# Kernel tuning notes

Measured on AMD Instinct MI355X. Metric: run time of the kernel, lower is better.

The kernel has to match this reference:

```python
import jax, jax.numpy as jnp
import numpy as np

LN_EPS = 1e-5

def setup_inputs() -> dict:
    key = jax.random.key(0)
    ks = jax.random.split(key, 6)
    B, S, Hid = 8, 8, 4096
    H, D = 32, 128
    MAX = 4096
    return {
        "tokens": jax.random.normal(ks[0], (B, S, Hid), jnp.float32),
        "cache_k": jax.random.normal(ks[1], (B, MAX, H, D), jnp.float32),
        "cache_v": jax.random.normal(ks[2], (B, MAX, H, D), jnp.float32),
        "ln_gamma": jnp.ones((Hid,), jnp.float32),
        "ln_beta": jnp.zeros((Hid,), jnp.float32),
        "qkv_w": jax.random.normal(ks[3], (3 * Hid, Hid), jnp.float32) * (Hid ** -0.5),
        "qkv_b": jnp.zeros((3 * Hid,), jnp.float32),
        "proj_w": jax.random.normal(ks[4], (Hid, Hid), jnp.float32) * (Hid ** -0.5),
        "proj_b": jnp.zeros((Hid,), jnp.float32),
        "start_offset": 4088,
    }

def reference(tokens, cache_k, cache_v, ln_gamma, ln_beta, qkv_w, qkv_b, proj_w, proj_b, start_offset):
    B, S, Hid = tokens.shape
    H = 32
    D = Hid // H
    scale = D ** -0.5
    # LayerNorm
    mu = jnp.mean(tokens, axis=-1, keepdims=True)
    var = jnp.mean(jnp.square(tokens - mu), axis=-1, keepdims=True)
    x = (tokens - mu) * jax.lax.rsqrt(var + LN_EPS) * ln_gamma + ln_beta
    # Fused QKV projection (torch Linear: y = x @ W^T + b)
    qkv = x @ qkv_w.T + qkv_b                      # [B, S, 3*Hid]
    qkv = qkv.reshape(B, S, 3, H, D)
    q, k, v = qkv[:, :, 0], qkv[:, :, 1], qkv[:, :, 2]   # each [B, S, H, D]
    # Append into KV cache (static offset -> lax slice update)
    cache_k = jax.lax.dynamic_update_slice_in_dim(cache_k, k, start_offset, axis=1)
    cache_v = jax.lax.dynamic_update_slice_in_dim(cache_v, v, start_offset, axis=1)
    T = start_offset + S
    k_ctx = cache_k[:, :T]                         # [B, T, H, D]
    v_ctx = cache_v[:, :T]
    # SDPA: thin query over full context, non-causal
    scores = jnp.einsum('bshd,bthd->bhst', q, k_ctx) * scale   # [B, H, S, T]
    attn = jax.nn.softmax(scores, axis=-1)
    out = jnp.einsum('bhst,bthd->bshd', attn, v_ctx).reshape(B, S, Hid)
    return out @ proj_w.T + proj_b
```

## Files before the change

### kernel.cpp

```cpp
#include <hip/hip_runtime.h>
#include <math.h>

#define HID 4096
#define NH 32
#define HD 128
#define BB 8
#define SS 8
#define MM 64
#define MAXT 4096
#define QKV_N (3*HID)
#define KSPLIT 4
#define CHUNK 1024
#define NCHUNK (MAXT/CHUNK)
#define TILE 32
#define NTILES (CHUNK/TILE)
#define CHUNK_STRIDE 260
#define KBUF_FLOATS (16*CHUNK_STRIDE)
#define GBK 64
#define ASTR 72

typedef __attribute__((ext_vector_type(8))) __bf16 bf16x8;
typedef __attribute__((ext_vector_type(4))) float f32x4;

__device__ __forceinline__ float wred_sum(float v) {
#pragma unroll
    for (int i = 1; i < 64; i <<= 1) v += __shfl_xor(v, i, 64);
    return v;
}
__device__ __forceinline__ float hred_sum(float v) {
#pragma unroll
    for (int i = 1; i < 32; i <<= 1) v += __shfl_xor(v, i, 64);
    return v;
}
__device__ __forceinline__ float hred_max(float v) {
#pragma unroll
    for (int i = 1; i < 32; i <<= 1) v = fmaxf(v, __shfl_xor(v, i, 64));
    return v;
}

__global__ __launch_bounds__(256)
void ln_kernel(const float* __restrict__ tokens, const float* __restrict__ gamma,
               const float* __restrict__ beta, float* __restrict__ xout) {
    const int row = blockIdx.x;
    const float* in = tokens + (size_t)row * HID;
    float* out = xout + (size_t)row * HID;
    const int tid = threadIdx.x;
    float s = 0.f, s2 = 0.f;
    float4 vals[4];
#pragma unroll
    for (int i = 0; i < 4; ++i) {
        float4 v = *(const float4*)(in + (size_t)(i*256 + tid)*4);
        vals[i] = v;
        s  += v.x + v.y + v.z + v.w;
        s2 += v.x*v.x + v.y*v.y + v.z*v.z + v.w*v.w;
    }
    s = wred_sum(s); s2 = wred_sum(s2);
    __shared__ float red[8];
    int wid = tid >> 6, lane = tid & 63;
    if (lane == 0) { red[wid] = s; red[4+wid] = s2; }
    __syncthreads();
    s  = red[0]+red[1]+red[2]+red[3];
    s2 = red[4]+red[5]+red[6]+red[7];
    float mean = s * (1.f/HID);
    float var  = s2 * (1.f/HID) - mean*mean;
    float rstd = rsqrtf(var + 1e-5f);
#pragma unroll
    for (int i = 0; i < 4; ++i) {
        int base = (i*256 + tid)*4;
        float4 v = vals[i];
        float4 g  = *(const float4*)(gamma + base);
        float4 bt = *(const float4*)(beta + base);
        float4 o;
        o.x = (v.x - mean)*rstd*g.x + bt.x;
        o.y = (v.y - mean)*rstd*g.y + bt.y;
        o.z = (v.z - mean)*rstd*g.z + bt.z;
        o.w = (v.w - mean)*rstd*g.w + bt.w;
        *(float4*)(out + base) = o;
    }
}

__global__ __launch_bounds__(256, 2)
void gemm_mfma(const float* __restrict__ x, const float* __restrict__ w,
               float* __restrict__ part, int N, int K) {
    __shared__ __bf16 a_hi[64*ASTR], a_lo[64*ASTR];
    __shared__ __bf16 b_hi[64*ASTR], b_lo[64*ASTR];
    const int n0 = blockIdx.x * 64;
    const int kc = blockIdx.y;
    const int kLen = K / KSPLIT;
    const int kBeg = kc * kLen;
    const int tid = threadIdx.x;
    const int wv = tid >> 6;
    const int lane = tid & 63;
    const int wm = (wv & 1) * 32;
    const int wn = (wv >> 1) * 32;
    const int sr = tid >> 2;
    const int sk = (tid & 3) * 16;
    const int fm = lane & 15;
    const int fk = (lane >> 4) * 8;

    f32x4 acc[2][2] = {};
    const float* xsrc = x + (size_t)sr * K + kBeg + sk;
    const float* wsrc = w + (size_t)(n0 + sr) * K + kBeg + sk;

    float aRg[16], bRg[16];
#pragma unroll
    for (int q = 0; q < 4; ++q) {
        *(float4*)&aRg[q*4] = *(const float4*)(xsrc + q*4);
        *(float4*)&bRg[q*4] = *(const float4*)(wsrc + q*4);
    }
    const int nsteps = kLen / GBK;
    for (int st = 0; st < nsteps; ++st) {
        __syncthreads();
#pragma unroll
        for (int q = 0; q < 2; ++q) {
            bf16x8 ah, al, bh, bl;
#pragma unroll
            for (int j = 0; j < 8; ++j) {
                float av = aRg[q*8+j];
                __bf16 h = (__bf16)av;
                ah[j] = h;
                al[j] = (__bf16)(av - (float)h);
                float bv = bRg[q*8+j];
                __bf16 g = (__bf16)bv;
                bh[j] = g;
                bl[j] = (__bf16)(bv - (float)g);
            }
            int base = sr*ASTR + sk + q*8;
            *(bf16x8*)&a_hi[base] = ah;
            *(bf16x8*)&a_lo[base] = al;
            *(bf16x8*)&b_hi[base] = bh;
            *(bf16x8*)&b_lo[base] = bl;
        }
        __syncthreads();
        if (st + 1 < nsteps) {
            const float* xn = xsrc + (size_t)(st+1)*GBK;
            const float* wn_ = wsrc + (size_t)(st+1)*GBK;
#pragma unroll
            for (int q = 0; q < 4; ++q) {
                *(float4*)&aRg[q*4] = *(const float4*)(xn + q*4);
                *(float4*)&bRg[q*4] = *(const float4*)(wn_ + q*4);
            }
        }
#pragma unroll
        for (int kh = 0; kh < 2; ++kh) {
            bf16x8 Ah[2], Al[2], Bh[2], Bl[2];
#pragma unroll
            for (int t = 0; t < 2; ++t) {
                int ar = (wm + t*16 + fm)*ASTR + kh*32 + fk;
                Ah[t] = *(const bf16x8*)&a_hi[ar];
                Al[t] = *(const bf16x8*)&a_lo[ar];
                int br = (wn + t*16 + fm)*ASTR + kh*32 + fk;
                Bh[t] = *(const bf16x8*)&b_hi[br];
                Bl[t] = *(const bf16x8*)&b_lo[br];
            }
#pragma unroll
            for (int mt = 0; mt < 2; ++mt)
#pragma unroll
            for (int nt = 0; nt < 2; ++nt) {
                acc[mt][nt] = __builtin_amdgcn_mfma_f32_16x16x32_bf16(Ah[mt], Bh[nt], acc[mt][nt], 0, 0, 0);
                acc[mt][nt] = __builtin_amdgcn_mfma_f32_16x16x32_bf16(Ah[mt], Bl[nt], acc[mt][nt], 0, 0, 0);
                acc[mt][nt] = __builtin_amdgcn_mfma_f32_16x16x32_bf16(Al[mt], Bh[nt], acc[mt][nt], 0, 0, 0);
            }
        }
    }
    float* dst = part + (size_t)kc * MM * N;
#pragma unroll
    for (int mt = 0; mt < 2; ++mt)
#pragma unroll
    for (int nt = 0; nt < 2; ++nt) {
        int m = wm + mt*16 + (lane >> 4)*4;
        int n = n0 + wn + nt*16 + (lane & 15);
#pragma unroll
        for (int r = 0; r < 4; ++r)
            dst[(size_t)(m + r) * N + n] = acc[mt][nt][r];
    }
}

__global__ __launch_bounds__(256)
void combine_bias(const float* __restrict__ part, const float* __restrict__ bias,
                  float* __restrict__ out, int N, int totalv4) {
    int idx = blockIdx.x * 256 + threadIdx.x;
    if (idx >= totalv4) return;
    size_t base = (size_t)idx * 4;
    size_t MN = (size_t)MM * N;
    float4 a = *(const float4*)(part + base);
    float4 b = *(const float4*)(part + MN + base);
    float4 c = *(const float4*)(part + 2*MN + base);
    float4 d = *(const float4*)(part + 3*MN + base);
    int n = (int)(base % (size_t)N);
    float4 bb = *(const float4*)(bias + n);
    float4 o;
    o.x = a.x+b.x+c.x+d.x+bb.x;
    o.y = a.y+b.y+c.y+d.y+bb.y;
    o.z = a.z+b.z+c.z+d.z+bb.z;
    o.w = a.w+b.w+c.w+d.w+bb.w;
    *(float4*)(out + base) = o;
}

__global__ __launch_bounds__(256, 4)
void attn_part(const float* __restrict__ qkv, const float* __restrict__ cache_k,
               const float* __restrict__ cache_v, const int* __restrict__ d_start,
               float* __restrict__ accp, float* __restrict__ mlp) {
    __shared__ float k_lds[2*KBUF_FLOATS];
    __shared__ float q_lds[SS*HD];
    __shared__ float p_lds[SS*TILE];
    const int bh = blockIdx.x;
    const int b = bh >> 5, h = bh & 31;
    const int c = blockIdx.y;
    const int tid = threadIdx.x;
    const int start = d_start[0];
    const int T = start + SS;
    const float scale = 0.08838834764831845f;

    {
        int s_ = tid >> 5, dg = tid & 31;
        *(float4*)&q_lds[s_*HD + dg*4] =
            *(const float4*)(qkv + (size_t)(b*SS + s_)*QKV_N + h*HD + dg*4);
    }
    const int ts   = tid & 31;
    const int s    = tid >> 5;
    const int wave = tid >> 6;
    const int lane = tid & 63;
    const int hi   = lane >> 5;
    const int li   = lane & 31;

    const size_t cacheRowBase = ((size_t)b*MAXT*NH + h) * (size_t)HD;

    auto stage_tile = [&](int tbase, int buf) {
        float* base = k_lds + buf*KBUF_FLOATS;
#pragma unroll
        for (int j = 0; j < 4; ++j) {
            int ck = wave*4 + j;
            int tg = tbase + 2*ck + hi;
            const float* src = ((tg >= start && tg < T)
                ? (qkv + (size_t)(b*SS + (tg-start))*QKV_N + h*HD + HID)
                : (cache_k + cacheRowBase + (size_t)tg*NH*HD)) + li*4;
            __builtin_amdgcn_global_load_lds(
                (const __attribute__((address_space(1))) void*)src,
                (__attribute__((address_space(3))) void*)(base + ck*CHUNK_STRIDE),
                16, 0, 0);
        }
    };

    float m_r = -1e30f, l_r = 0.f;
    float4 oacc = make_float4(0.f,0.f,0.f,0.f);
    const int cbase = c*CHUNK;

    stage_tile(cbase, 0);
    asm volatile("s_waitcnt vmcnt(0)" ::: "memory");
    __syncthreads();

    int buf = 0;
    for (int tile = 0; tile < NTILES; ++tile) {
        const int tbase = cbase + tile*TILE;
        if (tile + 1 < NTILES) stage_tile(tbase + TILE, buf ^ 1);

        const float* kb = k_lds + buf*KBUF_FLOATS + (ts>>1)*CHUNK_STRIDE + (ts&1)*HD;
        const float* qrow = q_lds + s*HD;
        float d0 = 0.f;
#pragma unroll
        for (int dg = 0; dg < 32; ++dg) {
            float4 kv = *(const float4*)(kb + dg*4);
            float4 qa = *(const float4*)(qrow + dg*4);
            d0 += kv.x*qa.x + kv.y*qa.y + kv.z*qa.z + kv.w*qa.w;
        }
        int tg = tbase + ts;
        float sc = (tg < T) ? d0 * scale : -1e30f;
        float mt = hred_max(sc);
        float mn = fmaxf(m_r, mt);
        float al = __expf(m_r - mn);
        float p  = (tg < T) ? __expf(sc - mn) : 0.f;
        l_r = l_r * al + hred_sum(p);
        m_r = mn;
        p_lds[s*TILE + ts] = p;
        oacc.x *= al; oacc.y *= al; oacc.z *= al; oacc.w *= al;
        if (tbase + TILE <= start) {
            const float* vb = cache_v + cacheRowBase + (size_t)tbase*NH*HD + ts*4;
#pragma unroll 16
            for (int t2 = 0; t2 < TILE; ++t2) {
                float4 vv = *(const float4*)(vb + (size_t)t2*NH*HD);
                float pp = p_lds[s*TILE + t2];
                oacc.x += pp*vv.x; oacc.y += pp*vv.y; oacc.z += pp*vv.z; oacc.w += pp*vv.w;
            }
        } else {
#pragma unroll 8
            for (int t2 = 0; t2 < TILE; ++t2) {
                int tg2 = tbase + t2;
                const float* vrow = ((tg2 >= start && tg2 < T)
                    ? (qkv + (size_t)(b*SS + (tg2-start))*QKV_N + h*HD + 2*HID)
                    : (cache_v + cacheRowBase + (size_t)tg2*NH*HD));
                float4 vv = *(const float4*)(vrow + ts*4);
                float pp = p_lds[s*TILE + t2];
                oacc.x += pp*vv.x; oacc.y += pp*vv.y; oacc.z += pp*vv.z; oacc.w += pp*vv.w;
            }
        }
        asm volatile("s_waitcnt vmcnt(0)" ::: "memory");
        __syncthreads();
        buf ^= 1;
    }

    size_t pbase = ((size_t)(bh*NCHUNK + c) * SS + s) * HD + ts*4;
    *(float4*)(accp + pbase) = oacc;
    if (ts == 0) {
        size_t mb = (size_t)(bh*NCHUNK + c) * 16;
        mlp[mb + s] = m_r;
        mlp[mb + 8 + s] = l_r;
    }
}

__global__ __launch_bounds__(256)
void attn_combine(const float* __restrict__ accp, const float* __restrict__ mlp,
                  float* __restrict__ attn_out) {
    const int bh = blockIdx.x;
    const int b = bh >> 5, h = bh & 31;
    const int tid = threadIdx.x;
    const int s = tid >> 5, dg = tid & 31;
    float mC[NCHUNK], lC[NCHUNK];
    float M = -1e30f;
#pragma unroll
    for (int c = 0; c < NCHUNK; ++c) {
        size_t mb = (size_t)(bh*NCHUNK + c) * 16;
        mC[c] = mlp[mb + s];
        lC[c] = mlp[mb + 8 + s];
        M = fmaxf(M, mC[c]);
    }
    float L = 0.f;
    float4 o = make_float4(0.f,0.f,0.f,0.f);
#pragma unroll
    for (int c = 0; c < NCHUNK; ++c) {
        float wgt = __expf(mC[c] - M);
        L += wgt * lC[c];
        float4 a = *(const float4*)(accp + ((size_t)(bh*NCHUNK + c) * SS + s) * HD + dg*4);
        o.x += wgt*a.x; o.y += wgt*a.y; o.z += wgt*a.z; o.w += wgt*a.w;
    }
    float inv = 1.f / L;
    o.x *= inv; o.y *= inv; o.z *= inv; o.w *= inv;
    *(float4*)(attn_out + (size_t)(b*SS + s)*HID + h*HD + dg*4) = o;
}

extern "C" void kernel_launch(void* const* d_in, const int* in_sizes, int n_in,
                              void* d_out, int out_size, void* d_ws, size_t ws_size,
                              hipStream_t stream) {
    const float* tokens  = (const float*)d_in[0];
    const float* cache_k = (const float*)d_in[1];
    const float* cache_v = (const float*)d_in[2];
    const float* gamma   = (const float*)d_in[3];
    const float* beta    = (const float*)d_in[4];
    const float* qkv_w   = (const float*)d_in[5];
    const float* qkv_b   = (const float*)d_in[6];
    const float* proj_w  = (const float*)d_in[7];
    const float* proj_b  = (const float*)d_in[8];
    const int*   d_start = (const int*)d_in[9];
    float* out = (float*)d_out;
    char* ws = (char*)d_ws;

    float* x_ln     = (float*)ws;
    float* qkv      = (float*)(ws + (1u<<20));
    float* part     = (float*)(ws + (4u<<20));
    float* accp     = (float*)(ws + (4u<<20));
    float* mlp      = (float*)(ws + (12u<<20));
    float* attn_out = (float*)(ws + (16u<<20));

    ln_kernel<<<MM, 256, 0, stream>>>(tokens, gamma, beta, x_ln);
    gemm_mfma<<<dim3(QKV_N/64, KSPLIT), 256, 0, stream>>>(x_ln, qkv_w, part, QKV_N, HID);
    combine_bias<<<(MM*QKV_N/4 + 255)/256, 256, 0, stream>>>(part, qkv_b, qkv, QKV_N, MM*QKV_N/4);
    attn_part<<<dim3(BB*NH, NCHUNK), 256, 0, stream>>>(qkv, cache_k, cache_v, d_start, accp, mlp);
    attn_combine<<<BB*NH, 256, 0, stream>>>(accp, mlp, attn_out);
    gemm_mfma<<<dim3(HID/64, KSPLIT), 256, 0, stream>>>(attn_out, proj_w, part, HID, HID);
    combine_bias<<<(MM*HID/4 + 255)/256, 256, 0, stream>>>(part, proj_b, out, HID, MM*HID/4);
}
```

Before: 345.1 us.

## Rewrite attention partial kernel with bf16 MFMA for QK and PV

Replaces the scalar fp32 dot-product attention with bf16 MFMA 16x16x32 instructions for both QK^T scores and P·V accumulation. K and V tiles are loaded into registers, converted to bf16, and written to LDS (V transposed), with the next tile's global load overlapping compute. Chunk size doubles to 2048 and each wave keeps its own online-softmax partial, so the combine kernel now merges 4 partials per chunk. Q, K, V and P are rounded to bf16, which loses precision, and the grid has half as many blocks.

```diff
diff --git a/kernel.cpp b/kernel.cpp
--- a/kernel.cpp
+++ b/kernel.cpp
@@ -10,31 +10,25 @@
 #define MAXT 4096
 #define QKV_N (3*HID)
 #define KSPLIT 4
-#define CHUNK 1024
-#define NCHUNK (MAXT/CHUNK)
-#define TILE 32
-#define NTILES (CHUNK/TILE)
-#define CHUNK_STRIDE 260
-#define KBUF_FLOATS (16*CHUNK_STRIDE)
 #define GBK 64
 #define ASTR 72
 
+#define ATILE 64
+#define ACHUNK 2048
+#define NCHUNK (MAXT/ACHUNK)
+#define NTILES (ACHUNK/ATILE)
+#define NPART (NCHUNK*4)
+#define KSTR 136
+#define VSTR 88
+#define PSTR 136
+
 typedef __attribute__((ext_vector_type(8))) __bf16 bf16x8;
+typedef __attribute__((ext_vector_type(4))) __bf16 bf16x4;
 typedef __attribute__((ext_vector_type(4))) float f32x4;
 
 __device__ __forceinline__ float wred_sum(float v) {
 #pragma unroll
     for (int i = 1; i < 64; i <<= 1) v += __shfl_xor(v, i, 64);
-    return v;
-}
-__device__ __forceinline__ float hred_sum(float v) {
-#pragma unroll
-    for (int i = 1; i < 32; i <<= 1) v += __shfl_xor(v, i, 64);
-    return v;
-}
-__device__ __forceinline__ float hred_max(float v) {
-#pragma unroll
-    for (int i = 1; i < 32; i <<= 1) v = fmaxf(v, __shfl_xor(v, i, 64));
     return v;
 }
 
@@ -197,115 +191,165 @@
     *(float4*)(out + base) = o;
 }
 
-__global__ __launch_bounds__(256, 4)
+__global__ __launch_bounds__(256)
 void attn_part(const float* __restrict__ qkv, const float* __restrict__ cache_k,
                const float* __restrict__ cache_v, const int* __restrict__ d_start,
                float* __restrict__ accp, float* __restrict__ mlp) {
-    __shared__ float k_lds[2*KBUF_FLOATS];
-    __shared__ float q_lds[SS*HD];
-    __shared__ float p_lds[SS*TILE];
+    __shared__ __bf16 k_lds[ATILE*KSTR];
+    __shared__ __bf16 v_lds[HD*VSTR];
+    __shared__ __bf16 p_lds[16*PSTR];
     const int bh = blockIdx.x;
     const int b = bh >> 5, h = bh & 31;
     const int c = blockIdx.y;
     const int tid = threadIdx.x;
+    const int w = tid >> 6;
+    const int lane = tid & 63;
+    const int l15 = lane & 15;
+    const int lg  = lane >> 4;
+    const int woff = w * 16;
     const int start = d_start[0];
     const int T = start + SS;
     const float scale = 0.08838834764831845f;
 
+    const int d4 = (tid & 31) * 4;
+    const int tq = tid >> 5;
+
+    const size_t cacheRowBase = ((size_t)b*MAXT*NH + h) * (size_t)HD;
+    const int cbase = c * ACHUNK;
+
+    float4 kreg[8], vreg[8];
+#define LOAD_TILE(TB)                                                             \
+    {                                                                             \
+        _Pragma("unroll")                                                         \
+        for (int j = 0; j < 8; ++j) {                                             \
+            int tg = (TB) + tq*8 + j;                                             \
+            bool fresh = (tg >= start) && (tg < T);                               \
+            const float* kp = fresh                                               \
+                ? (qkv + (size_t)(b*SS + (tg-start))*QKV_N + h*HD + HID)          \
+                : (cache_k + cacheRowBase + (size_t)tg*NH*HD);                    \
+            const float* vp = fresh                                               \
+                ? (qkv + (size_t)(b*SS + (tg-start))*QKV_N + h*HD + 2*HID)        \
+                : (cache_v + cacheRowBase + (size_t)tg*NH*HD);                    \
+            kreg[j] = *(const float4*)(kp + d4);                                  \
+            vreg[j] = *(const float4*)(vp + d4);                                  \
+        }                                                                         \
+    }
+
+    bf16x8 qf[4];
+    if (l15 < SS) {
+        const float* qp = qkv + (size_t)(b*SS + l15)*QKV_N + h*HD + lg*8;
+#pragma unroll
+        for (int ks = 0; ks < 4; ++ks) {
+            float4 a = *(const float4*)(qp + ks*32);
+            float4 b2 = *(const float4*)(qp + ks*32 + 4);
+            bf16x8 q8;
+            q8[0]=(__bf16)a.x;  q8[1]=(__bf16)a.y;  q8[2]=(__bf16)a.z;  q8[3]=(__bf16)a.w;
+            q8[4]=(__bf16)b2.x; q8[5]=(__bf16)b2.y; q8[6]=(__bf16)b2.z; q8[7]=(__bf16)b2.w;
+            qf[ks] = q8;
+        }
+    } else {
+#pragma unroll
+        for (int ks = 0; ks < 4; ++ks) qf[ks] = (bf16x8)(__bf16)0.0f;
+    }
     {
-        int s_ = tid >> 5, dg = tid & 31;
-        *(float4*)&q_lds[s_*HD + dg*4] =
-            *(const float4*)(qkv + (size_t)(b*SS + s_)*QKV_N + h*HD + dg*4);
-    }
-    const int ts   = tid & 31;
-    const int s    = tid >> 5;
-    const int wave = tid >> 6;
-    const int lane = tid & 63;
-    const int hi   = lane >> 5;
-    const int li   = lane & 31;
-
-    const size_t cacheRowBase = ((size_t)b*MAXT*NH + h) * (size_t)HD;
-
-    auto stage_tile = [&](int tbase, int buf) {
-        float* base = k_lds + buf*KBUF_FLOATS;
-#pragma unroll
-        for (int j = 0; j < 4; ++j) {
-            int ck = wave*4 + j;
-            int tg = tbase + 2*ck + hi;
-            const float* src = ((tg >= start && tg < T)
-                ? (qkv + (size_t)(b*SS + (tg-start))*QKV_N + h*HD + HID)
-                : (cache_k + cacheRowBase + (size_t)tg*NH*HD)) + li*4;
-            __builtin_amdgcn_global_load_lds(
-                (const __attribute__((address_space(1))) void*)src,
-                (__attribute__((address_space(3))) void*)(base + ck*CHUNK_STRIDE),
-                16, 0, 0);
-        }
-    };
+        int zs = tid & 15;
+        int zw = (tid >> 4) & 3;
+        int zj = tid >> 6;
+        *(bf16x4*)&p_lds[zs*PSTR + zw*32 + 16 + zj*4] = (bf16x4)(__bf16)0.0f;
+    }
+    {
+        int zr = tid & 127;
+        int zc = 64 + (tid >> 7) * 8;
+        *(bf16x8*)&v_lds[zr*VSTR + zc] = (bf16x8)(__bf16)0.0f;
+    }
+    LOAD_TILE(cbase);
+    __syncthreads();
 
     float m_r = -1e30f, l_r = 0.f;
-    float4 oacc = make_float4(0.f,0.f,0.f,0.f);
-    const int cbase = c*CHUNK;
-
-    stage_tile(cbase, 0);
-    asm volatile("s_waitcnt vmcnt(0)" ::: "memory");
-    __syncthreads();
-
-    int buf = 0;
+    f32x4 oacc[8] = {};
+
     for (int tile = 0; tile < NTILES; ++tile) {
-        const int tbase = cbase + tile*TILE;
-        if (tile + 1 < NTILES) stage_tile(tbase + TILE, buf ^ 1);
-
-        const float* kb = k_lds + buf*KBUF_FLOATS + (ts>>1)*CHUNK_STRIDE + (ts&1)*HD;
-        const float* qrow = q_lds + s*HD;
-        float d0 = 0.f;
-#pragma unroll
-        for (int dg = 0; dg < 32; ++dg) {
-            float4 kv = *(const float4*)(kb + dg*4);
-            float4 qa = *(const float4*)(qrow + dg*4);
-            d0 += kv.x*qa.x + kv.y*qa.y + kv.z*qa.z + kv.w*qa.w;
-        }
-        int tg = tbase + ts;
-        float sc = (tg < T) ? d0 * scale : -1e30f;
-        float mt = hred_max(sc);
-        float mn = fmaxf(m_r, mt);
+        const int tbase = cbase + tile*ATILE;
+#pragma unroll
+        for (int j = 0; j < 8; ++j) {
+            bf16x4 kb;
+            kb[0]=(__bf16)kreg[j].x; kb[1]=(__bf16)kreg[j].y;
+            kb[2]=(__bf16)kreg[j].z; kb[3]=(__bf16)kreg[j].w;
+            *(bf16x4*)&k_lds[(tq*8+j)*KSTR + d4] = kb;
+        }
+#pragma unroll
+        for (int i = 0; i < 4; ++i) {
+            bf16x8 vt;
+#pragma unroll
+            for (int j = 0; j < 8; ++j)
+                vt[j] = (__bf16)(((const float*)&vreg[j])[i]);
+            *(bf16x8*)&v_lds[(d4 + i)*VSTR + tq*8] = vt;
+        }
+        __syncthreads();
+        if (tile + 1 < NTILES) LOAD_TILE(tbase + ATILE);
+
+        f32x4 sacc = {0.f, 0.f, 0.f, 0.f};
+#pragma unroll
+        for (int ks = 0; ks < 4; ++ks) {
+            bf16x8 kf = *(const bf16x8*)&k_lds[(woff + l15)*KSTR + ks*32 + lg*8];
+            sacc = __builtin_amdgcn_mfma_f32_16x16x32_bf16(kf, qf[ks], sacc, 0, 0, 0);
+        }
+        float sc[4]; bool val[4];
+#pragma unroll
+        for (int r = 0; r < 4; ++r) {
+            int tg = tbase + woff + lg*4 + r;
+            val[r] = tg < T;
+            sc[r] = val[r] ? sacc[r]*scale : -1e30f;
+        }
+        float tmax = fmaxf(fmaxf(sc[0], sc[1]), fmaxf(sc[2], sc[3]));
+        tmax = fmaxf(tmax, __shfl_xor(tmax, 16, 64));
+        tmax = fmaxf(tmax, __shfl_xor(tmax, 32, 64));
+        float mn = fmaxf(m_r, tmax);
         float al = __expf(m_r - mn);
-        float p  = (tg < T) ? __expf(sc - mn) : 0.f;
-        l_r = l_r * al + hred_sum(p);
+        float p[4];
+#pragma unroll
+        for (int r = 0; r < 4; ++r) p[r] = val[r] ? __expf(sc[r] - mn) : 0.f;
+        float psum = (p[0]+p[1]) + (p[2]+p[3]);
+        psum += __shfl_xor(psum, 16, 64);
+        psum += __shfl_xor(psum, 32, 64);
+        l_r = l_r * al + psum;
         m_r = mn;
-        p_lds[s*TILE + ts] = p;
-        oacc.x *= al; oacc.y *= al; oacc.z *= al; oacc.w *= al;
-        if (tbase + TILE <= start) {
-            const float* vb = cache_v + cacheRowBase + (size_t)tbase*NH*HD + ts*4;
-#pragma unroll 16
-            for (int t2 = 0; t2 < TILE; ++t2) {
-                float4 vv = *(const float4*)(vb + (size_t)t2*NH*HD);
-                float pp = p_lds[s*TILE + t2];
-                oacc.x += pp*vv.x; oacc.y += pp*vv.y; oacc.z += pp*vv.z; oacc.w += pp*vv.w;
-            }
-        } else {
-#pragma unroll 8
-            for (int t2 = 0; t2 < TILE; ++t2) {
-                int tg2 = tbase + t2;
-                const float* vrow = ((tg2 >= start && tg2 < T)
-                    ? (qkv + (size_t)(b*SS + (tg2-start))*QKV_N + h*HD + 2*HID)
-                    : (cache_v + cacheRowBase + (size_t)tg2*NH*HD));
-                float4 vv = *(const float4*)(vrow + ts*4);
-                float pp = p_lds[s*TILE + t2];
-                oacc.x += pp*vv.x; oacc.y += pp*vv.y; oacc.z += pp*vv.z; oacc.w += pp*vv.w;
-            }
-        }
-        asm volatile("s_waitcnt vmcnt(0)" ::: "memory");
+        bf16x4 pb;
+        pb[0]=(__bf16)p[0]; pb[1]=(__bf16)p[1]; pb[2]=(__bf16)p[2]; pb[3]=(__bf16)p[3];
+        *(bf16x4*)&p_lds[l15*PSTR + w*32 + lg*4] = pb;
+        float als[4];
+#pragma unroll
+        for (int r = 0; r < 4; ++r) als[r] = __shfl(al, lg*4 + r, 64);
+#pragma unroll
+        for (int dt = 0; dt < 8; ++dt) {
+            oacc[dt][0] *= als[0]; oacc[dt][1] *= als[1];
+            oacc[dt][2] *= als[2]; oacc[dt][3] *= als[3];
+        }
+        bf16x8 pa = *(const bf16x8*)&p_lds[l15*PSTR + w*32 + lg*8];
+#pragma unroll
+        for (int dt = 0; dt < 8; ++dt) {
+            bf16x8 vb = *(const bf16x8*)&v_lds[(dt*16 + l15)*VSTR + woff + lg*8];
+            oacc[dt] = __builtin_amdgcn_mfma_f32_16x16x32_bf16(pa, vb, oacc[dt], 0, 0, 0);
+        }
         __syncthreads();
-        buf ^= 1;
-    }
-
-    size_t pbase = ((size_t)(bh*NCHUNK + c) * SS + s) * HD + ts*4;
-    *(float4*)(accp + pbase) = oacc;
-    if (ts == 0) {
-        size_t mb = (size_t)(bh*NCHUNK + c) * 16;
-        mlp[mb + s] = m_r;
-        mlp[mb + 8 + s] = l_r;
-    }
+    }
+
+    const int pidx = (bh*NCHUNK + c)*4 + w;
+    float* abase = accp + (size_t)pidx * SS * HD;
+#pragma unroll
+    for (int r = 0; r < 4; ++r) {
+        int s = lg*4 + r;
+        if (s < SS) {
+#pragma unroll
+            for (int dt = 0; dt < 8; ++dt)
+                abase[(size_t)s*HD + dt*16 + l15] = oacc[dt][r];
+        }
+    }
+    if (lane < SS) {
+        mlp[(size_t)pidx*16 + lane] = m_r;
+        mlp[(size_t)pidx*16 + 8 + lane] = l_r;
+    }
+#undef LOAD_TILE
 }
 
 __global__ __launch_bounds__(256)
@@ -315,22 +359,22 @@
     const int b = bh >> 5, h = bh & 31;
     const int tid = threadIdx.x;
     const int s = tid >> 5, dg = tid & 31;
-    float mC[NCHUNK], lC[NCHUNK];
+    float mC[NPART], lC[NPART];
     float M = -1e30f;
 #pragma unroll
-    for (int c = 0; c < NCHUNK; ++c) {
-        size_t mb = (size_t)(bh*NCHUNK + c) * 16;
-        mC[c] = mlp[mb + s];
-        lC[c] = mlp[mb + 8 + s];
-        M = fmaxf(M, mC[c]);
+    for (int p = 0; p < NPART; ++p) {
+        size_t mb = (size_t)(bh*NPART + p) * 16;
+        mC[p] = mlp[mb + s];
+        lC[p] = mlp[mb + 8 + s];
+        M = fmaxf(M, mC[p]);
     }
     float L = 0.f;
     float4 o = make_float4(0.f,0.f,0.f,0.f);
 #pragma unroll
-    for (int c = 0; c < NCHUNK; ++c) {
-        float wgt = __expf(mC[c] - M);
-        L += wgt * lC[c];
-        float4 a = *(const float4*)(accp + ((size_t)(bh*NCHUNK + c) * SS + s) * HD + dg*4);
+    for (int p = 0; p < NPART; ++p) {
+        float wgt = __expf(mC[p] - M);
+        L += wgt * lC[p];
+        float4 a = *(const float4*)(accp + ((size_t)(bh*NPART + p) * SS + s) * HD + dg*4);
         o.x += wgt*a.x; o.y += wgt*a.y; o.z += wgt*a.z; o.w += wgt*a.w;
     }
     float inv = 1.f / L;
```

Result: faster. 298.0 us (-13.6%).
